# Kernel optimization log

Hardware: AMD Instinct MI355X
Metric: run time of the kernel (lower is better)

## Reference

```python
import jax, jax.numpy as jnp
import numpy as np

WIN = 1024   # win_length == n_fft
HOP = 256    # win_length // 4
NFFT = 1024
B = 8
T = 2000     # frames


def setup_inputs() -> dict:
    key = jax.random.key(0)
    z = jax.random.normal(key, (B, 2 * (NFFT // 2 + 1), T), dtype=jnp.float32)
    n = jnp.arange(WIN, dtype=jnp.float32)
    window = 0.54 - 0.46 * jnp.cos(2.0 * jnp.pi * n / WIN)
    return {"z": z, "window": window}


def reference(z, window):
    b, c, t = z.shape
    f = c // 2
    # first half of channels = real, second half = imag; -> [b, t, f] complex
    zc = jnp.transpose(z[:, :f] + 1j * z[:, f:], (0, 2, 1))
    # unnormalized-onesided inverse (old torch.irfft, normalized=False) == np irfft
    sig = jnp.fft.irfft(zc, n=NFFT, axis=-1)[..., :WIN].astype(z.dtype) * window
    # overlap-add (the conv_transpose1d with eye kernel is exactly a scatter-add)
    L = (t - 1) * HOP + WIN
    idx = (jnp.arange(t) * HOP)[:, None] + jnp.arange(WIN)
    ola = jnp.zeros((b, L), sig.dtype).at[:, idx].add(sig)
    wnorm = jnp.zeros((L,), sig.dtype).at[idx].add(
        jnp.broadcast_to(window * window, (t, WIN)))
    half = WIN // 2
    return ola[:, half:L - half] / wnorm[half:L - half]
```

## Files before the change

kernel.cpp:

```cpp
#include <hip/hip_runtime.h>


#define TFRAMES 2000
#define NB 8
#define LOUT 511744
#define PI_F 3.14159265358979323846f
#define YW_BYTES ((size_t)NB * TFRAMES * 512 * 2 * sizeof(float))

__global__ __launch_bounds__(256) void build_yprime(const float* __restrict__ z,
                                                    float* __restrict__ yw) {
  __shared__ float tA[32][33];
  __shared__ float tB[32][33];
  __shared__ float tC[32][33];
  __shared__ float tD[32][33];
  const int b  = blockIdx.z;
  const int k0 = blockIdx.y * 32;
  const int t0 = blockIdx.x * 32;
  const int tid = threadIdx.x;
  const int tt = tid & 31;
  const int rg = tid >> 5;
  const float* zb = z + (size_t)b * 1026 * TFRAMES;
  const int t = t0 + tt;
  const bool tin = (t < TFRAMES);
  for (int rr = rg; rr < 32; rr += 8) {
    tA[rr][tt] = tin ? zb[(size_t)(k0 + rr) * TFRAMES + t] : 0.f;
    tB[rr][tt] = tin ? zb[(size_t)(512 - k0 - 31 + rr) * TFRAMES + t] : 0.f;
    tC[rr][tt] = tin ? zb[(size_t)(513 + k0 + rr) * TFRAMES + t] : 0.f;
    tD[rr][tt] = tin ? zb[(size_t)(1025 - k0 - 31 + rr) * TFRAMES + t] : 0.f;
  }
  __syncthreads();
  const int kk = tid & 31;
  const int k = k0 + kk;
  float s, c;
  sincosf(PI_F * (float)k / 512.0f, &s, &c);
  for (int tr = rg; tr < 32; tr += 8) {
    int tcur = t0 + tr;
    if (tcur >= TFRAMES) break;
    float xr  = tA[kk][tr];
    float xr2 = tB[31 - kk][tr];
    float xi  = tC[kk][tr];
    float xi2 = tD[31 - kk][tr];
    if (k == 0) { xi = 0.f; xi2 = 0.f; }
    float Ar = xr + xr2;
    float Ai = xi - xi2;
    float Brp = xr - xr2;
    float Bip = xi + xi2;
    float Br = Brp * c - Bip * s;
    float Bi = Brp * s + Bip * c;
    float2 o = make_float2(Ar - Bi, Ai + Br);
    reinterpret_cast<float2*>(yw)[((size_t)b * TFRAMES + tcur) * 512 + k] = o;
  }
}

__device__ __forceinline__ float2 cadd(float2 a, float2 b) {
  return make_float2(a.x + b.x, a.y + b.y);
}
__device__ __forceinline__ float2 csub(float2 a, float2 b) {
  return make_float2(a.x - b.x, a.y - b.y);
}
__device__ __forceinline__ float2 cmul(float2 a, float2 b) {
  return make_float2(a.x * b.x - a.y * b.y, a.x * b.y + a.y * b.x);
}
__device__ __forceinline__ float2 cmuli(float2 a) {
  return make_float2(-a.y, a.x);
}

__device__ __forceinline__ void dft8(const float2* x, float2* y) {
  const float S = 0.70710678118654752440f;
  float2 t0 = cadd(x[0], x[4]), t1 = csub(x[0], x[4]);
  float2 t2 = cadd(x[2], x[6]), t3 = csub(x[2], x[6]);
  float2 t4 = cadd(x[1], x[5]), t5 = csub(x[1], x[5]);
  float2 t6 = cadd(x[3], x[7]), t7 = csub(x[3], x[7]);
  float2 it3 = cmuli(t3);
  float2 E0 = cadd(t0, t2), E2 = csub(t0, t2);
  float2 E1 = cadd(t1, it3), E3 = csub(t1, it3);
  float2 it7 = cmuli(t7);
  float2 O0 = cadd(t4, t6), O2 = csub(t4, t6);
  float2 O1 = cadd(t5, it7), O3 = csub(t5, it7);
  float2 w1O = make_float2(S * (O1.x - O1.y), S * (O1.x + O1.y));
  float2 w2O = cmuli(O2);
  float2 w3O = make_float2(-S * (O3.x + O3.y), S * (O3.x - O3.y));
  y[0] = cadd(E0, O0); y[4] = csub(E0, O0);
  y[1] = cadd(E1, w1O); y[5] = csub(E1, w1O);
  y[2] = cadd(E2, w2O); y[6] = csub(E2, w2O);
  y[3] = cadd(E3, w3O); y[7] = csub(E3, w3O);
}

__global__ __launch_bounds__(64) void ifft8_frames(float* __restrict__ ws,
                                                   const float* __restrict__ win) {
  __shared__ float2 sh[584];
  const int tid = threadIdx.x;
  const int frame = blockIdx.x;
  float2* fr = reinterpret_cast<float2*>(ws) + (size_t)frame * 512;
  const float2* win2 = reinterpret_cast<const float2*>(win);

  float2 x[8], y[8];
#pragma unroll
  for (int j = 0; j < 8; ++j) x[j] = fr[tid + 64 * j];

  dft8(x, y);
  {
    float s1, c1;
    sincosf((2.0f * PI_F / 512.0f) * (float)tid, &s1, &c1);
    float2 w = make_float2(c1, s1);
    float2 cur = w;
    y[1] = cmul(y[1], cur);
#pragma unroll
    for (int j = 2; j < 8; ++j) { cur = cmul(cur, w); y[j] = cmul(y[j], cur); }
  }
  const int row1 = (tid & 7) * 8 + (tid >> 3);
#pragma unroll
  for (int j = 0; j < 8; ++j) sh[row1 * 9 + j] = y[j];
  __syncthreads();

  {
    const int k1 = tid & 7, j1 = tid >> 3;
#pragma unroll
    for (int k2 = 0; k2 < 8; ++k2) x[k2] = sh[(k1 * 8 + k2) * 9 + j1];
    dft8(x, y);
    float s1, c1;
    sincosf((2.0f * PI_F / 64.0f) * (float)k1, &s1, &c1);
    float2 w = make_float2(c1, s1);
    float2 cur = w;
    y[1] = cmul(y[1], cur);
#pragma unroll
    for (int j = 2; j < 8; ++j) { cur = cmul(cur, w); y[j] = cmul(y[j], cur); }
    __syncthreads();
#pragma unroll
    for (int j2 = 0; j2 < 8; ++j2) sh[(j1 * 8 + j2) * 9 + k1] = y[j2];
  }
  __syncthreads();

#pragma unroll
  for (int k1 = 0; k1 < 8; ++k1) x[k1] = sh[row1 * 9 + k1];
  dft8(x, y);

  const float scale = 1.0f / 1024.0f;
#pragma unroll
  for (int j3 = 0; j3 < 8; ++j3) {
    const int m = tid + 64 * j3;
    const float2 wv = win2[m];
    fr[m] = make_float2(y[j3].x * wv.x * scale, y[j3].y * wv.y * scale);
  }
}

__global__ __launch_bounds__(256) void gather_norm(const float* __restrict__ frames,
                                                   const float* __restrict__ win,
                                                   float* __restrict__ out) {
  const int b = blockIdx.y;
  const int q = blockIdx.x * 256 + threadIdx.x;
  const int p = q + 512;
  const int tb = p >> 8;
  const int pm = p & 255;
  const float* fb = frames + (size_t)b * TFRAMES * 1024;
  float acc = 0.f, wn = 0.f;
#pragma unroll
  for (int j = 0; j < 4; ++j) {
    const int t = tb - j;
    if (t >= 0 && t < TFRAMES) {
      const int o = pm + (j << 8);
      acc += fb[(size_t)t * 1024 + o];
      const float w = win[o];
      wn += w * w;
    }
  }
  out[(size_t)b * LOUT + q] = acc / wn;
}

__device__ __forceinline__ void fft_ola_tail(float* ar, float* ai, float* br,
                                             float* bi, const float* twc,
                                             const float* tws,
                                             const float* __restrict__ win,
                                             float* __restrict__ out, int b,
                                             int t, int tid) {
  for (int sstage = 0; sstage < 9; ++sstage) {
    const int m = 1 << sstage;
    for (int u = 0; u < 4; ++u) {
      const int i = tid + (u << 6);
      const float xar = ar[i],       xai = ai[i];
      const float xbr = ar[i + 256], xbi = ai[i + 256];
      const int h = i & ~(m - 1);
      const int idx = i + h;
      br[idx] = xar + xbr;
      bi[idx] = xai + xbi;
      const float tr = xar - xbr;
      const float ti = xai - xbi;
      const float c = twc[h], sn = tws[h];
      br[idx + m] = tr * c - ti * sn;
      bi[idx + m] = tr * sn + ti * c;
    }
    __syncthreads();
    float* tmp;
    tmp = ar; ar = br; br = tmp;
    tmp = ai; ai = bi; bi = tmp;
  }
  const float scale = 1.0f / 1024.0f;
  const size_t obase = (size_t)b * LOUT;
  const int pbase = t * 256 - 512;
  for (int i = tid; i < 512; i += 64) {
    const float v0 = ar[i] * scale * win[2 * i];
    const float v1 = ai[i] * scale * win[2 * i + 1];
    const int p0 = pbase + 2 * i;
    const int p1 = p0 + 1;
    if (p0 >= 0 && p0 < LOUT) atomicAdd(&out[obase + p0], v0);
    if (p1 >= 0 && p1 < LOUT) atomicAdd(&out[obase + p1], v1);
  }
}

__global__ __launch_bounds__(64) void ifft_ola_fused(const float* __restrict__ z,
                                                     const float* __restrict__ win,
                                                     float* __restrict__ out) {
  __shared__ float Zr[513];
  __shared__ float Zi[513];
  __shared__ float Xr[512];
  __shared__ float Xi[512];
  __shared__ float Yr[512];
  __shared__ float Yi[512];
  __shared__ float twc[256];
  __shared__ float tws[256];
  const int tid = threadIdx.x;
  const int frame = blockIdx.x;
  const int b = frame / TFRAMES;
  const int t = frame - b * TFRAMES;
  const float* zb = z + (size_t)b * 1026 * TFRAMES + t;
  for (int r = tid; r < 513; r += 64) {
    Zr[r] = zb[(size_t)r * TFRAMES];
    Zi[r] = zb[(size_t)(513 + r) * TFRAMES];
  }
  for (int r = tid; r < 256; r += 64) {
    float s, c;
    sincosf((PI_F / 256.0f) * (float)r, &s, &c);
    twc[r] = c; tws[r] = s;
  }
  __syncthreads();
  for (int k = tid; k < 512; k += 64) {
    float xr  = Zr[k];
    float xr2 = Zr[512 - k];
    float xi  = (k == 0) ? 0.f : Zi[k];
    float xi2 = (k == 0) ? 0.f : Zi[512 - k];
    float s, c;
    sincosf(PI_F * (float)k / 512.0f, &s, &c);
    float Ar = xr + xr2;
    float Ai = xi - xi2;
    float Brp = xr - xr2;
    float Bip = xi + xi2;
    float Br = Brp * c - Bip * s;
    float Bi = Brp * s + Bip * c;
    Xr[k] = Ar - Bi;
    Xi[k] = Ai + Br;
  }
  __syncthreads();
  fft_ola_tail(Xr, Xi, Yr, Yi, twc, tws, win, out, b, t, tid);
}

__global__ __launch_bounds__(256) void normalize_kernel(const float* __restrict__ win,
                                                        float* __restrict__ out) {
  const int total = NB * LOUT;
  for (int idx = blockIdx.x * blockDim.x + threadIdx.x; idx < total;
       idx += gridDim.x * blockDim.x) {
    const int q = idx % LOUT;
    const int p = q + 512;
    const int pm = p & 255;
    float wn = 0.f;
#pragma unroll
    for (int j = 0; j < 4; ++j) {
      const int o = pm + 256 * j;
      const int tt = (p - o) >> 8;
      if (tt >= 0 && tt < TFRAMES) {
        const float w = win[o];
        wn += w * w;
      }
    }
    out[idx] = out[idx] / wn;
  }
}

extern "C" void kernel_launch(void* const* d_in, const int* in_sizes, int n_in,
                              void* d_out, int out_size, void* d_ws, size_t ws_size,
                              hipStream_t stream) {
  const float* z   = (const float*)d_in[0];
  const float* win = (const float*)d_in[1];
  float* out = (float*)d_out;

  if (ws_size >= YW_BYTES) {
    float* yw = (float*)d_ws;
    dim3 gA((TFRAMES + 31) / 32, 512 / 32, NB);
    build_yprime<<<gA, 256, 0, stream>>>(z, yw);
    ifft8_frames<<<NB * TFRAMES, 64, 0, stream>>>(yw, win);
    dim3 gG(LOUT / 256, NB);
    gather_norm<<<gG, 256, 0, stream>>>(yw, win, out);
  } else {
    hipMemsetAsync(d_out, 0, (size_t)out_size * sizeof(float), stream);
    ifft_ola_fused<<<NB * TFRAMES, 64, 0, stream>>>(z, win, out);
    normalize_kernel<<<2048, 256, 0, stream>>>(win, out);
  }
}
```

Measured before the change: 156.3 us.

## Fuse spectrum packing into the per-frame iFFT kernel with 8 frames per block

Replaces the separate build_yprime transpose/pack kernel and the 64-thread ifft8_frames kernel with a single kernel. Each 512-thread block loads 8 frames' worth of spectrum columns from z into shared memory, packs the half-size complex sequence in registers, and runs the 512-point radix-8 FFT with one wave per frame. Twiddles come from a constant table times one sincos. This removes a full write and re-read of the intermediate spectrum buffer and one launch. In exchange it uses about 37KB of shared memory per block, and the z loads are only 8-byte-wide strided reads per row.

```diff
diff --git a/kernel.cpp b/kernel.cpp
--- a/kernel.cpp
+++ b/kernel.cpp
@@ -6,51 +6,7 @@
 #define LOUT 511744
 #define PI_F 3.14159265358979323846f
 #define YW_BYTES ((size_t)NB * TFRAMES * 512 * 2 * sizeof(float))
-
-__global__ __launch_bounds__(256) void build_yprime(const float* __restrict__ z,
-                                                    float* __restrict__ yw) {
-  __shared__ float tA[32][33];
-  __shared__ float tB[32][33];
-  __shared__ float tC[32][33];
-  __shared__ float tD[32][33];
-  const int b  = blockIdx.z;
-  const int k0 = blockIdx.y * 32;
-  const int t0 = blockIdx.x * 32;
-  const int tid = threadIdx.x;
-  const int tt = tid & 31;
-  const int rg = tid >> 5;
-  const float* zb = z + (size_t)b * 1026 * TFRAMES;
-  const int t = t0 + tt;
-  const bool tin = (t < TFRAMES);
-  for (int rr = rg; rr < 32; rr += 8) {
-    tA[rr][tt] = tin ? zb[(size_t)(k0 + rr) * TFRAMES + t] : 0.f;
-    tB[rr][tt] = tin ? zb[(size_t)(512 - k0 - 31 + rr) * TFRAMES + t] : 0.f;
-    tC[rr][tt] = tin ? zb[(size_t)(513 + k0 + rr) * TFRAMES + t] : 0.f;
-    tD[rr][tt] = tin ? zb[(size_t)(1025 - k0 - 31 + rr) * TFRAMES + t] : 0.f;
-  }
-  __syncthreads();
-  const int kk = tid & 31;
-  const int k = k0 + kk;
-  float s, c;
-  sincosf(PI_F * (float)k / 512.0f, &s, &c);
-  for (int tr = rg; tr < 32; tr += 8) {
-    int tcur = t0 + tr;
-    if (tcur >= TFRAMES) break;
-    float xr  = tA[kk][tr];
-    float xr2 = tB[31 - kk][tr];
-    float xi  = tC[kk][tr];
-    float xi2 = tD[31 - kk][tr];
-    if (k == 0) { xi = 0.f; xi2 = 0.f; }
-    float Ar = xr + xr2;
-    float Ai = xi - xi2;
-    float Brp = xr - xr2;
-    float Bip = xi + xi2;
-    float Br = Brp * c - Bip * s;
-    float Bi = Brp * s + Bip * c;
-    float2 o = make_float2(Ar - Bi, Ai + Br);
-    reinterpret_cast<float2*>(yw)[((size_t)b * TFRAMES + tcur) * 512 + k] = o;
-  }
-}
+#define NT 8
 
 __device__ __forceinline__ float2 cadd(float2 a, float2 b) {
   return make_float2(a.x + b.x, a.y + b.y);
@@ -86,41 +42,86 @@
   y[3] = cadd(E3, w3O); y[7] = csub(E3, w3O);
 }
 
-__global__ __launch_bounds__(64) void ifft8_frames(float* __restrict__ ws,
-                                                   const float* __restrict__ win) {
-  __shared__ float2 sh[584];
-  const int tid = threadIdx.x;
-  const int frame = blockIdx.x;
-  float2* fr = reinterpret_cast<float2*>(ws) + (size_t)frame * 512;
-  const float2* win2 = reinterpret_cast<const float2*>(win);
-
+__global__ __launch_bounds__(512, 4) void pack_fft_frames(
+    const float* __restrict__ z, const float* __restrict__ win,
+    float* __restrict__ frames) {
+  __shared__ __attribute__((aligned(16))) unsigned char smem[37376];
+  float*  sz      = reinterpret_cast<float*>(smem);
+  float2* scratch = reinterpret_cast<float2*>(smem);
+  const int tid  = threadIdx.x;
+  const int lane = tid & 63;
+  const int wave = tid >> 6;
+  const int b    = blockIdx.y;
+  const int t0   = blockIdx.x * NT;
+  const float* zb = z + (size_t)b * 1026 * TFRAMES;
+
+#pragma unroll
+  for (int pass = 0; pass < 9; ++pass) {
+    const int r = pass * 128 + (tid >> 2);
+    if (r < 1026) {
+      const int tq = (tid & 3) * 2;
+      const float2 v = *reinterpret_cast<const float2*>(
+          zb + (size_t)r * TFRAMES + (t0 + tq));
+      sz[tq * 1026 + r]       = v.x;
+      sz[(tq + 1) * 1026 + r] = v.y;
+    }
+  }
+  __syncthreads();
+
+  const float* szt = sz + wave * 1026;
   float2 x[8], y[8];
-#pragma unroll
-  for (int j = 0; j < 8; ++j) x[j] = fr[tid + 64 * j];
+  float s0, c0;
+  sincosf(PI_F * (float)lane / 512.0f, &s0, &c0);
+  const float2 w0 = make_float2(c0, s0);
+  const float2 W16[8] = {
+    { 1.f, 0.f},
+    { 0.92387953251128675613f, 0.38268343236508977173f},
+    { 0.70710678118654752440f, 0.70710678118654752440f},
+    { 0.38268343236508977173f, 0.92387953251128675613f},
+    { 0.f, 1.f},
+    {-0.38268343236508977173f, 0.92387953251128675613f},
+    {-0.70710678118654752440f, 0.70710678118654752440f},
+    {-0.92387953251128675613f, 0.38268343236508977173f}};
+#pragma unroll
+  for (int q = 0; q < 8; ++q) {
+    const int k = q * 64 + lane;
+    const float xr  = szt[k];
+    const float xr2 = szt[512 - k];
+    float xi  = szt[513 + k];
+    float xi2 = szt[1025 - k];
+    if (k == 0) { xi = 0.f; xi2 = 0.f; }
+    const float2 tw = cmul(W16[q], w0);
+    const float Ar = xr + xr2,  Ai = xi - xi2;
+    const float Brp = xr - xr2, Bip = xi + xi2;
+    const float Br = Brp * tw.x - Bip * tw.y;
+    const float Bi = Brp * tw.y + Bip * tw.x;
+    x[q] = make_float2(Ar - Bi, Ai + Br);
+  }
+  __syncthreads();
+
+  float2* sh = scratch + wave * 584;
 
   dft8(x, y);
   {
-    float s1, c1;
-    sincosf((2.0f * PI_F / 512.0f) * (float)tid, &s1, &c1);
-    float2 w = make_float2(c1, s1);
-    float2 cur = w;
+    const float2 w1 = cmul(w0, w0);
+    float2 cur = w1;
     y[1] = cmul(y[1], cur);
 #pragma unroll
-    for (int j = 2; j < 8; ++j) { cur = cmul(cur, w); y[j] = cmul(y[j], cur); }
-  }
-  const int row1 = (tid & 7) * 8 + (tid >> 3);
+    for (int j = 2; j < 8; ++j) { cur = cmul(cur, w1); y[j] = cmul(y[j], cur); }
+  }
+  const int row1 = (lane & 7) * 8 + (lane >> 3);
 #pragma unroll
   for (int j = 0; j < 8; ++j) sh[row1 * 9 + j] = y[j];
   __syncthreads();
 
   {
-    const int k1 = tid & 7, j1 = tid >> 3;
+    const int k1 = lane & 7, j1 = lane >> 3;
 #pragma unroll
     for (int k2 = 0; k2 < 8; ++k2) x[k2] = sh[(k1 * 8 + k2) * 9 + j1];
     dft8(x, y);
     float s1, c1;
     sincosf((2.0f * PI_F / 64.0f) * (float)k1, &s1, &c1);
-    float2 w = make_float2(c1, s1);
+    const float2 w = make_float2(c1, s1);
     float2 cur = w;
     y[1] = cmul(y[1], cur);
 #pragma unroll
@@ -136,9 +137,13 @@
   dft8(x, y);
 
   const float scale = 1.0f / 1024.0f;
+  const int t = t0 + wave;
+  float2* fr = reinterpret_cast<float2*>(frames) +
+               ((size_t)b * TFRAMES + t) * 512;
+  const float2* win2 = reinterpret_cast<const float2*>(win);
 #pragma unroll
   for (int j3 = 0; j3 < 8; ++j3) {
-    const int m = tid + 64 * j3;
+    const int m = lane + 64 * j3;
     const float2 wv = win2[m];
     fr[m] = make_float2(y[j3].x * wv.x * scale, y[j3].y * wv.y * scale);
   }
@@ -283,12 +288,11 @@
   float* out = (float*)d_out;
 
   if (ws_size >= YW_BYTES) {
-    float* yw = (float*)d_ws;
-    dim3 gA((TFRAMES + 31) / 32, 512 / 32, NB);
-    build_yprime<<<gA, 256, 0, stream>>>(z, yw);
-    ifft8_frames<<<NB * TFRAMES, 64, 0, stream>>>(yw, win);
+    float* frames = (float*)d_ws;
+    dim3 gA(TFRAMES / NT, NB);
+    pack_fft_frames<<<gA, 512, 0, stream>>>(z, win, frames);
     dim3 gG(LOUT / 256, NB);
-    gather_norm<<<gG, 256, 0, stream>>>(yw, win, out);
+    gather_norm<<<gG, 256, 0, stream>>>(frames, win, out);
   } else {
     hipMemsetAsync(d_out, 0, (size_t)out_size * sizeof(float), stream);
     ifft_ola_fused<<<NB * TFRAMES, 64, 0, stream>>>(z, win, out);
```

After: 144.6 us. 7.5% less time.
